# Optimization experiments

Measured on AMD Instinct MI355X. Metric: run time of the kernel, lower is better.

Reference implementation:

```python
import jax, jax.numpy as jnp
import numpy as np

NUM_HEAD = 16
FEAT_DIM = 1024
HEAD_DIM = FEAT_DIM // NUM_HEAD  # 64
MAX_SEQ_LEN = 2048
BATCH = 2


def setup_inputs() -> dict:
    key = jax.random.key(0)
    ks = jax.random.split(key, 6)
    x = jax.random.normal(ks[0], (BATCH, MAX_SEQ_LEN, FEAT_DIM), dtype=jnp.float32)
    # xavier_uniform: limit = sqrt(6/(fan_in+fan_out)); torch Linear weight is [out, in]
    def xavier(k, out_f, in_f):
        lim = float(np.sqrt(6.0 / (in_f + out_f)))
        return jax.random.uniform(k, (out_f, in_f), dtype=jnp.float32, minval=-lim, maxval=lim)
    W1 = xavier(ks[1], HEAD_DIM, HEAD_DIM)          # attn_mlp[0].weight
    b1 = jnp.zeros((HEAD_DIM,), dtype=jnp.float32)
    W2 = xavier(ks[2], MAX_SEQ_LEN, HEAD_DIM)       # attn_mlp[2].weight
    b2 = jnp.zeros((MAX_SEQ_LEN,), dtype=jnp.float32)
    Wv = xavier(ks[3], FEAT_DIM, FEAT_DIM)          # value_linear.weight (no bias)
    Wo = xavier(ks[4], FEAT_DIM, FEAT_DIM)          # output_linear.weight (no bias)
    return {"x": x, "W1": W1, "b1": b1, "W2": W2, "b2": b2, "Wv": Wv, "Wo": Wo}


def _split_head(t):
    b, n, _ = t.shape
    return t.reshape(b, n, NUM_HEAD, HEAD_DIM).transpose(0, 2, 1, 3)  # [b,h,n,d]


def reference(x, W1, b1, W2, b2, Wv, Wo):
    # value projection (dropout is identity in eval / p=0)
    value = x @ Wv.T                                   # [b,n,F]
    vh = _split_head(value)                            # [b,h,n,d]
    xh = _split_head(x)                                # [b,h,n,d]
    # per-head MLP -> dense attention logits [b,h,n,max_seq_len]
    hid = jax.nn.relu(jnp.einsum('bhnd,ed->bhne', xh, W1) + b1)
    logits = jnp.einsum('bhne,me->bhnm', hid, W2) + b2
    attn = jax.nn.softmax(logits, axis=-1)             # [b,h,n,m]
    out_h = jnp.einsum('bhnm,bhmd->bhnd', attn, vh)    # m == seq_len
    b_, h_, n_, d_ = out_h.shape
    out = out_h.transpose(0, 2, 1, 3).reshape(b_, n_, FEAT_DIM)
    return out @ Wo.T
```

## Files before the change

kernel.cpp:

```cpp
#include <hip/hip_runtime.h>
#include <hip/hip_bf16.h>
#include <math.h>
#include <stdint.h>


typedef __attribute__((ext_vector_type(8))) short bf16x8;
typedef __attribute__((ext_vector_type(4))) float f32x4;

#define LOG2E 1.4426950408889634f

__device__ __forceinline__ unsigned short f2bf(float f) {
  union { float f; unsigned u; } v; v.f = f;
  unsigned r = v.u + 0x7FFFu + ((v.u >> 16) & 1u);
  return (unsigned short)(r >> 16);
}

__global__ __launch_bounds__(256) void conv_bf16(const float* __restrict__ src,
                                                 unsigned short* __restrict__ dst, int nq) {
  int stride = gridDim.x * blockDim.x;
  for (int q = blockIdx.x * blockDim.x + threadIdx.x; q < nq; q += stride) {
    float4 v = *(const float4*)(src + (size_t)q * 4);
    unsigned short p0 = f2bf(v.x), p1 = f2bf(v.y), p2 = f2bf(v.z), p3 = f2bf(v.w);
    uint2 u;
    u.x = (unsigned)p0 | ((unsigned)p1 << 16);
    u.y = (unsigned)p2 | ((unsigned)p3 << 16);
    *(uint2*)(dst + (size_t)q * 4) = u;
  }
}

__global__ __launch_bounds__(256) void b2l_kernel(const float* __restrict__ src,
                                                  float* __restrict__ dst, int n) {
  int i = blockIdx.x * blockDim.x + threadIdx.x;
  if (i < n) dst[i] = src[i] * LOG2E;
}

__device__ __forceinline__ void stage64(const char* g, size_t ldbytes, char* lds,
                                        int w, int lane) {
#pragma unroll
  for (int t = 0; t < 2; ++t) {
    int row  = w * 16 + t * 8 + (lane >> 3);
    int csrc = (lane & 7) ^ (lane >> 3);
    const char* src = g + (size_t)row * ldbytes + (csrc << 4);
    char* dst = lds + ((w * 2 + t) << 10);
    __builtin_amdgcn_global_load_lds((const __attribute__((address_space(1))) void*)src,
                                     (__attribute__((address_space(3))) void*)dst,
                                     16, 0, 0);
  }
}

__device__ __forceinline__ bf16x8 rdfrag(const char* lds, int row, int kt, int lane) {
  int c = ((kt << 2) + (lane >> 4)) ^ (row & 7);
  return *(const bf16x8*)(lds + row * 128 + (c << 4));
}

template<int MODE>
__global__ __launch_bounds__(256) void gemm_bt(const unsigned short* __restrict__ A,
                                               const unsigned short* __restrict__ B,
                                               void* __restrict__ C, int K) {
  __shared__ __attribute__((aligned(16))) char As[8192];
  __shared__ __attribute__((aligned(16))) char Bs[8192];
  int tid = threadIdx.x, w = tid >> 6, lane = tid & 63;
  int bm = blockIdx.x, bn = blockIdx.y;
  const char* Ab = (const char*)A + (size_t)bm * 64 * (K * 2);
  const char* Bb = (const char*)B + (size_t)bn * 64 * (K * 2);
  f32x4 acc[4] = {};
  int nsteps = K >> 6;
  for (int kk = 0; kk < nsteps; ++kk) {
    __syncthreads();
    stage64(Ab + (size_t)kk * 128, (size_t)K * 2, As, w, lane);
    stage64(Bb + (size_t)kk * 128, (size_t)K * 2, Bs, w, lane);
    __syncthreads();
#pragma unroll
    for (int kt = 0; kt < 2; ++kt) {
      bf16x8 a = rdfrag(As, w * 16 + (lane & 15), kt, lane);
#pragma unroll
      for (int nj = 0; nj < 4; ++nj) {
        bf16x8 b = rdfrag(Bs, nj * 16 + (lane & 15), kt, lane);
        acc[nj] = __builtin_amdgcn_mfma_f32_16x16x32_bf16(a, b, acc[nj], 0, 0, 0);
      }
    }
  }
  int g = lane >> 4, fr = lane & 15;
  if (MODE == 0) {
    unsigned short* vt = (unsigned short*)C;
    int growbase = bm * 64 + w * 16 + g * 4;
    int b = growbase >> 11;
    int n = growbase & 2047;
#pragma unroll
    for (int nj = 0; nj < 4; ++nj) {
      int d = nj * 16 + fr;
      unsigned short p0 = f2bf(acc[nj][0]), p1 = f2bf(acc[nj][1]);
      unsigned short p2 = f2bf(acc[nj][2]), p3 = f2bf(acc[nj][3]);
      uint2 u;
      u.x = (unsigned)p0 | ((unsigned)p1 << 16);
      u.y = (unsigned)p2 | ((unsigned)p3 << 16);
      *(uint2*)(vt + ((size_t)((b * 16 + bn) * 64 + d)) * 2048 + n) = u;
    }
  } else {
    float* Cf = (float*)C;
    int grow = bm * 64 + w * 16 + g * 4;
#pragma unroll
    for (int nj = 0; nj < 4; ++nj) {
#pragma unroll
      for (int r = 0; r < 4; ++r) {
        Cf[(size_t)(grow + r) * 1024 + bn * 64 + nj * 16 + fr] = acc[nj][r];
      }
    }
  }
}

__global__ __launch_bounds__(256) void flash_kernel(const unsigned short* __restrict__ xb,
                                                    const unsigned short* __restrict__ w1b,
                                                    const float* __restrict__ b1,
                                                    const unsigned short* __restrict__ w2b,
                                                    const float* __restrict__ b2l,
                                                    const unsigned short* __restrict__ vt,
                                                    unsigned short* __restrict__ aout) {
  __shared__ __attribute__((aligned(16))) char Ks[2][8192];
  __shared__ __attribute__((aligned(16))) char Vs[2][8192];
  __shared__ __attribute__((aligned(16))) char Qs[8192];
  int tid = threadIdx.x, w = tid >> 6, lane = tid & 63;
  int qt = blockIdx.x, bh = blockIdx.y;
  int b = bh >> 4, h = bh & 15;
  int g = lane >> 4, fr = lane & 15;

  stage64((const char*)(xb + ((size_t)(b * 2048 + qt * 64)) * 1024 + h * 64), 2048, Ks[0], w, lane);
  stage64((const char*)w1b, 128, Vs[0], w, lane);
  __syncthreads();
  {
    f32x4 hq[4] = {};
#pragma unroll
    for (int kt = 0; kt < 2; ++kt) {
      bf16x8 a = rdfrag(Ks[0], w * 16 + fr, kt, lane);
#pragma unroll
      for (int j = 0; j < 4; ++j) {
        bf16x8 bw = rdfrag(Vs[0], j * 16 + fr, kt, lane);
        hq[j] = __builtin_amdgcn_mfma_f32_16x16x32_bf16(a, bw, hq[j], 0, 0, 0);
      }
    }
#pragma unroll
    for (int r = 0; r < 4; ++r) {
      int row = w * 16 + g * 4 + r;
      int swz = (row & 7) << 4;
#pragma unroll
      for (int j = 0; j < 4; ++j) {
        float v = fmaxf(hq[j][r] + b1[j * 16 + fr], 0.f) * LOG2E;
        int byteoff = (row << 7) + ((((j << 4) + fr) << 1) ^ swz);
        *(unsigned short*)(Qs + byteoff) = f2bf(v);
      }
    }
  }
  bf16x8 qf0 = rdfrag(Qs, w * 16 + fr, 0, lane);
  bf16x8 qf1 = rdfrag(Qs, w * 16 + fr, 1, lane);
  __syncthreads();

  const char* vtb = (const char*)vt + (size_t)bh * 64 * 4096;
  stage64((const char*)w2b, 128, Ks[0], w, lane);
  stage64(vtb, 4096, Vs[0], w, lane);

  bf16x8 ones;
#pragma unroll
  for (int i = 0; i < 8; ++i) ones[i] = (short)0x3F80;

  f32x4 o[4] = {};
  f32x4 o1 = {};
  char* myPs = Qs + (w << 11);
  int cur = 0;
  int swz = (fr & 7) << 4;

  float4 e4a[4];
#pragma unroll
  for (int j = 0; j < 4; ++j) e4a[j] = *(const float4*)(b2l + j * 16 + g * 4);

  __syncthreads();

  for (int mt = 0; mt < 32; ++mt) {
    if (mt < 31) {
      stage64((const char*)w2b + (size_t)(mt + 1) * 8192, 128, Ks[cur ^ 1], w, lane);
      stage64(vtb + (size_t)(mt + 1) * 128, 4096, Vs[cur ^ 1], w, lane);
    }

    f32x4 s[4];
#pragma unroll
    for (int j = 0; j < 4; ++j) {
      s[j] = (f32x4){e4a[j].x, e4a[j].y, e4a[j].z, e4a[j].w};
      bf16x8 kb0 = rdfrag(Ks[cur], j * 16 + fr, 0, lane);
      s[j] = __builtin_amdgcn_mfma_f32_16x16x32_bf16(kb0, qf0, s[j], 0, 0, 0);
      bf16x8 kb1 = rdfrag(Ks[cur], j * 16 + fr, 1, lane);
      s[j] = __builtin_amdgcn_mfma_f32_16x16x32_bf16(kb1, qf1, s[j], 0, 0, 0);
    }
    if (mt < 31) {
#pragma unroll
      for (int j = 0; j < 4; ++j)
        e4a[j] = *(const float4*)(b2l + (mt + 1) * 64 + j * 16 + g * 4);
    }

#pragma unroll
    for (int j = 0; j < 4; ++j) {
      float p0, p1, p2, p3;
      asm("v_exp_f32 %0, %1" : "=v"(p0) : "v"(s[j][0]));
      asm("v_exp_f32 %0, %1" : "=v"(p1) : "v"(s[j][1]));
      asm("v_exp_f32 %0, %1" : "=v"(p2) : "v"(s[j][2]));
      asm("v_exp_f32 %0, %1" : "=v"(p3) : "v"(s[j][3]));
      unsigned ux, uy;
      asm("v_cvt_pk_bf16_f32 %0, %1, %2" : "=v"(ux) : "v"(p0), "v"(p1));
      asm("v_cvt_pk_bf16_f32 %0, %1, %2" : "=v"(uy) : "v"(p2), "v"(p3));
      uint2 u; u.x = ux; u.y = uy;
      int byteoff = (fr << 7) + (((j << 5) + (g << 3)) ^ swz);
      *(uint2*)(myPs + byteoff) = u;
    }

#pragma unroll
    for (int kt = 0; kt < 2; ++kt) {
      bf16x8 pf = rdfrag(myPs, fr, kt, lane);
      o1 = __builtin_amdgcn_mfma_f32_16x16x32_bf16(pf, ones, o1, 0, 0, 0);
#pragma unroll
      for (int dj = 0; dj < 4; ++dj) {
        bf16x8 vb = rdfrag(Vs[cur], dj * 16 + fr, kt, lane);
        o[dj] = __builtin_amdgcn_mfma_f32_16x16x32_bf16(pf, vb, o[dj], 0, 0, 0);
      }
    }
    __syncthreads();
    cur ^= 1;
  }

  float invr[4];
#pragma unroll
  for (int r = 0; r < 4; ++r) invr[r] = 1.f / o1[r];
  int nbase = qt * 64 + w * 16 + g * 4;
#pragma unroll
  for (int dj = 0; dj < 4; ++dj) {
    int f = h * 64 + dj * 16 + fr;
#pragma unroll
    for (int r = 0; r < 4; ++r) {
      aout[((size_t)(b * 2048 + nbase + r)) * 1024 + f] = f2bf(o[dj][r] * invr[r]);
    }
  }
}

extern "C" void kernel_launch(void* const* d_in, const int* in_sizes, int n_in,
                              void* d_out, int out_size, void* d_ws, size_t ws_size,
                              hipStream_t stream) {
  (void)in_sizes; (void)n_in; (void)out_size; (void)ws_size;
  const float* x  = (const float*)d_in[0];
  const float* W1 = (const float*)d_in[1];
  const float* b1 = (const float*)d_in[2];
  const float* W2 = (const float*)d_in[3];
  const float* b2 = (const float*)d_in[4];
  const float* Wv = (const float*)d_in[5];
  const float* Wo = (const float*)d_in[6];
  float* out = (float*)d_out;

  char* ws = (char*)d_ws;
  unsigned short* xb   = (unsigned short*)(ws);
  unsigned short* wvb  = (unsigned short*)(ws +  8388608);
  unsigned short* wob  = (unsigned short*)(ws + 10485760);
  unsigned short* w2b  = (unsigned short*)(ws + 12582912);
  unsigned short* w1b  = (unsigned short*)(ws + 12845056);
  float*          b2l  = (float*)         (ws + 12853248);
  unsigned short* vt   = (unsigned short*)(ws + 21233664);
  unsigned short* aout = (unsigned short*)(ws + 29622272);

  conv_bf16<<<1024, 256, 0, stream>>>(x,  xb,  4194304 / 4);
  conv_bf16<<<1024, 256, 0, stream>>>(Wv, wvb, 1048576 / 4);
  conv_bf16<<<1024, 256, 0, stream>>>(Wo, wob, 1048576 / 4);
  conv_bf16<<< 128, 256, 0, stream>>>(W2, w2b,  131072 / 4);
  conv_bf16<<<   4, 256, 0, stream>>>(W1, w1b,    4096 / 4);
  b2l_kernel<<<   8, 256, 0, stream>>>(b2, b2l, 2048);

  gemm_bt<0><<<dim3(64, 16), 256, 0, stream>>>(xb, wvb, (void*)vt, 1024);
  flash_kernel<<<dim3(32, 32), 256, 0, stream>>>(xb, w1b, b1, w2b, b2l, vt, aout);
  gemm_bt<1><<<dim3(64, 16), 256, 0, stream>>>(aout, wob, (void*)out, 1024);
}
```

Measured before the change: 113.7 us.

## Rewrite attention kernel with 32x32 MFMA, 128-row query tiles and register P

New measurement: 110.7 us. -2.7%, faster.

```diff
diff --git a/kernel.cpp b/kernel.cpp
--- a/kernel.cpp
+++ b/kernel.cpp
@@ -6,6 +6,7 @@
 
 typedef __attribute__((ext_vector_type(8))) short bf16x8;
 typedef __attribute__((ext_vector_type(4))) float f32x4;
+typedef __attribute__((ext_vector_type(16))) float f32x16;
 
 #define LOG2E 1.4426950408889634f
 
@@ -51,6 +52,35 @@
 __device__ __forceinline__ bf16x8 rdfrag(const char* lds, int row, int kt, int lane) {
   int c = ((kt << 2) + (lane >> 4)) ^ (row & 7);
   return *(const bf16x8*)(lds + row * 128 + (c << 4));
+}
+
+__device__ __forceinline__ bf16x8 rdfrag32(const char* lds, int row, int chunk) {
+  int c = chunk ^ (row & 7);
+  return *(const bf16x8*)(lds + row * 128 + (c << 4));
+}
+
+__device__ __forceinline__ f32x16 loadb16(const float* p) {
+  f32x16 r;
+#pragma unroll
+  for (int qd = 0; qd < 4; ++qd) {
+    float4 v = *(const float4*)(p + qd * 8);
+    r[qd * 4 + 0] = v.x; r[qd * 4 + 1] = v.y; r[qd * 4 + 2] = v.z; r[qd * 4 + 3] = v.w;
+  }
+  return r;
+}
+
+__device__ __forceinline__ bf16x8 pk_swap(float r0, float r1, float r2, float r3,
+                                          float r4, float r5, float r6, float r7) {
+  unsigned a, b, c, d;
+  asm("v_cvt_pk_bf16_f32 %0, %1, %2" : "=v"(a) : "v"(r0), "v"(r1));
+  asm("v_cvt_pk_bf16_f32 %0, %1, %2" : "=v"(b) : "v"(r4), "v"(r5));
+  asm("v_cvt_pk_bf16_f32 %0, %1, %2" : "=v"(c) : "v"(r2), "v"(r3));
+  asm("v_cvt_pk_bf16_f32 %0, %1, %2" : "=v"(d) : "v"(r6), "v"(r7));
+  asm("v_permlane32_swap_b32 %0, %1" : "+v"(a), "+v"(b));
+  asm("v_permlane32_swap_b32 %0, %1" : "+v"(c), "+v"(d));
+  union { unsigned u[4]; bf16x8 v; } r;
+  r.u[0] = a; r.u[1] = c; r.u[2] = b; r.u[3] = d;
+  return r.v;
 }
 
 template<int MODE>
@@ -116,125 +146,126 @@
                                                     const float* __restrict__ b2l,
                                                     const unsigned short* __restrict__ vt,
                                                     unsigned short* __restrict__ aout) {
-  __shared__ __attribute__((aligned(16))) char Ks[2][8192];
-  __shared__ __attribute__((aligned(16))) char Vs[2][8192];
-  __shared__ __attribute__((aligned(16))) char Qs[8192];
+  __shared__ __attribute__((aligned(16))) char Kbuf[16384];
+  __shared__ __attribute__((aligned(16))) char Vbuf[16384];
   int tid = threadIdx.x, w = tid >> 6, lane = tid & 63;
-  int qt = blockIdx.x, bh = blockIdx.y;
+  int l31 = lane & 31, hi = lane >> 5;
+  int f = blockIdx.x;
+  int swz = ((f & 7) << 6) | (f >> 3);
+  int qt = swz & 15, bh = swz >> 4;
   int b = bh >> 4, h = bh & 15;
-  int g = lane >> 4, fr = lane & 15;
-
-  stage64((const char*)(xb + ((size_t)(b * 2048 + qt * 64)) * 1024 + h * 64), 2048, Ks[0], w, lane);
-  stage64((const char*)w1b, 128, Vs[0], w, lane);
+
+  const char* px = (const char*)(xb + ((size_t)(b * 2048 + qt * 128)) * 1024 + h * 64);
+  stage64(px, 2048, Kbuf, w, lane);
+  stage64(px + (size_t)64 * 2048, 2048, Kbuf + 8192, w, lane);
+  stage64((const char*)w1b, 128, Vbuf, w, lane);
   __syncthreads();
-  {
-    f32x4 hq[4] = {};
-#pragma unroll
-    for (int kt = 0; kt < 2; ++kt) {
-      bf16x8 a = rdfrag(Ks[0], w * 16 + fr, kt, lane);
-#pragma unroll
-      for (int j = 0; j < 4; ++j) {
-        bf16x8 bw = rdfrag(Vs[0], j * 16 + fr, kt, lane);
-        hq[j] = __builtin_amdgcn_mfma_f32_16x16x32_bf16(a, bw, hq[j], 0, 0, 0);
+
+  f32x16 h0 = loadb16(b1 + hi * 4);
+  f32x16 h1 = loadb16(b1 + 32 + hi * 4);
+#pragma unroll
+  for (int ks = 0; ks < 4; ++ks) {
+    bf16x8 xf = rdfrag32(Kbuf, w * 32 + l31, ks * 2 + hi);
+    bf16x8 wf0 = rdfrag32(Vbuf, l31, ks * 2 + hi);
+    h0 = __builtin_amdgcn_mfma_f32_32x32x16_bf16(wf0, xf, h0, 0, 0, 0);
+    bf16x8 wf1 = rdfrag32(Vbuf, 32 + l31, ks * 2 + hi);
+    h1 = __builtin_amdgcn_mfma_f32_32x32x16_bf16(wf1, xf, h1, 0, 0, 0);
+  }
+#pragma unroll
+  for (int i = 0; i < 16; ++i) {
+    h0[i] = fmaxf(h0[i], 0.f) * LOG2E;
+    h1[i] = fmaxf(h1[i], 0.f) * LOG2E;
+  }
+  bf16x8 qb[4];
+  qb[0] = pk_swap(h0[0], h0[1], h0[2], h0[3], h0[4], h0[5], h0[6], h0[7]);
+  qb[1] = pk_swap(h0[8], h0[9], h0[10], h0[11], h0[12], h0[13], h0[14], h0[15]);
+  qb[2] = pk_swap(h1[0], h1[1], h1[2], h1[3], h1[4], h1[5], h1[6], h1[7]);
+  qb[3] = pk_swap(h1[8], h1[9], h1[10], h1[11], h1[12], h1[13], h1[14], h1[15]);
+  __syncthreads();
+
+  const char* vtb = (const char*)vt + (size_t)bh * 64 * 4096;
+  stage64((const char*)w2b, 128, Kbuf, w, lane);
+  stage64(vtb, 4096, Vbuf, w, lane);
+  float4 pre[8];
+#pragma unroll
+  for (int pq = 0; pq < 4; ++pq) {
+    pre[pq]     = *(const float4*)(b2l + pq * 8 + hi * 4);
+    pre[pq + 4] = *(const float4*)(b2l + 32 + pq * 8 + hi * 4);
+  }
+  f32x16 oA = {}, oB = {};
+  float lrs0 = 0.f, lrs1 = 0.f, lrs2 = 0.f, lrs3 = 0.f;
+  __syncthreads();
+
+  for (int mt = 0; mt < 32; ++mt) {
+    int cur = mt & 1;
+    const char* Kc = Kbuf + (cur << 13);
+    const char* Vc = Vbuf + (cur << 13);
+    if (mt < 31) {
+      stage64((const char*)w2b + (size_t)(mt + 1) * 8192, 128, Kbuf + ((cur ^ 1) << 13), w, lane);
+      stage64(vtb + (size_t)(mt + 1) * 128, 4096, Vbuf + ((cur ^ 1) << 13), w, lane);
+    }
+    f32x16 s0, s1;
+#pragma unroll
+    for (int qd = 0; qd < 4; ++qd) {
+      s0[qd * 4 + 0] = pre[qd].x;     s0[qd * 4 + 1] = pre[qd].y;
+      s0[qd * 4 + 2] = pre[qd].z;     s0[qd * 4 + 3] = pre[qd].w;
+      s1[qd * 4 + 0] = pre[qd + 4].x; s1[qd * 4 + 1] = pre[qd + 4].y;
+      s1[qd * 4 + 2] = pre[qd + 4].z; s1[qd * 4 + 3] = pre[qd + 4].w;
+    }
+#pragma unroll
+    for (int kt = 0; kt < 4; ++kt) {
+      bf16x8 kf0 = rdfrag32(Kc, l31, kt * 2 + hi);
+      s0 = __builtin_amdgcn_mfma_f32_32x32x16_bf16(kf0, qb[kt], s0, 0, 0, 0);
+      bf16x8 kf1 = rdfrag32(Kc, 32 + l31, kt * 2 + hi);
+      s1 = __builtin_amdgcn_mfma_f32_32x32x16_bf16(kf1, qb[kt], s1, 0, 0, 0);
+    }
+    if (mt < 31) {
+#pragma unroll
+      for (int pq = 0; pq < 4; ++pq) {
+        pre[pq]     = *(const float4*)(b2l + (mt + 1) * 64 + pq * 8 + hi * 4);
+        pre[pq + 4] = *(const float4*)(b2l + (mt + 1) * 64 + 32 + pq * 8 + hi * 4);
       }
     }
 #pragma unroll
-    for (int r = 0; r < 4; ++r) {
-      int row = w * 16 + g * 4 + r;
-      int swz = (row & 7) << 4;
-#pragma unroll
-      for (int j = 0; j < 4; ++j) {
-        float v = fmaxf(hq[j][r] + b1[j * 16 + fr], 0.f) * LOG2E;
-        int byteoff = (row << 7) + ((((j << 4) + fr) << 1) ^ swz);
-        *(unsigned short*)(Qs + byteoff) = f2bf(v);
-      }
-    }
-  }
-  bf16x8 qf0 = rdfrag(Qs, w * 16 + fr, 0, lane);
-  bf16x8 qf1 = rdfrag(Qs, w * 16 + fr, 1, lane);
-  __syncthreads();
-
-  const char* vtb = (const char*)vt + (size_t)bh * 64 * 4096;
-  stage64((const char*)w2b, 128, Ks[0], w, lane);
-  stage64(vtb, 4096, Vs[0], w, lane);
-
-  bf16x8 ones;
-#pragma unroll
-  for (int i = 0; i < 8; ++i) ones[i] = (short)0x3F80;
-
-  f32x4 o[4] = {};
-  f32x4 o1 = {};
-  char* myPs = Qs + (w << 11);
-  int cur = 0;
-  int swz = (fr & 7) << 4;
-
-  float4 e4a[4];
-#pragma unroll
-  for (int j = 0; j < 4; ++j) e4a[j] = *(const float4*)(b2l + j * 16 + g * 4);
-
-  __syncthreads();
-
-  for (int mt = 0; mt < 32; ++mt) {
-    if (mt < 31) {
-      stage64((const char*)w2b + (size_t)(mt + 1) * 8192, 128, Ks[cur ^ 1], w, lane);
-      stage64(vtb + (size_t)(mt + 1) * 128, 4096, Vs[cur ^ 1], w, lane);
-    }
-
-    f32x4 s[4];
-#pragma unroll
-    for (int j = 0; j < 4; ++j) {
-      s[j] = (f32x4){e4a[j].x, e4a[j].y, e4a[j].z, e4a[j].w};
-      bf16x8 kb0 = rdfrag(Ks[cur], j * 16 + fr, 0, lane);
-      s[j] = __builtin_amdgcn_mfma_f32_16x16x32_bf16(kb0, qf0, s[j], 0, 0, 0);
-      bf16x8 kb1 = rdfrag(Ks[cur], j * 16 + fr, 1, lane);
-      s[j] = __builtin_amdgcn_mfma_f32_16x16x32_bf16(kb1, qf1, s[j], 0, 0, 0);
-    }
-    if (mt < 31) {
-#pragma unroll
-      for (int j = 0; j < 4; ++j)
-        e4a[j] = *(const float4*)(b2l + (mt + 1) * 64 + j * 16 + g * 4);
-    }
-
-#pragma unroll
-    for (int j = 0; j < 4; ++j) {
-      float p0, p1, p2, p3;
-      asm("v_exp_f32 %0, %1" : "=v"(p0) : "v"(s[j][0]));
-      asm("v_exp_f32 %0, %1" : "=v"(p1) : "v"(s[j][1]));
-      asm("v_exp_f32 %0, %1" : "=v"(p2) : "v"(s[j][2]));
-      asm("v_exp_f32 %0, %1" : "=v"(p3) : "v"(s[j][3]));
-      unsigned ux, uy;
-      asm("v_cvt_pk_bf16_f32 %0, %1, %2" : "=v"(ux) : "v"(p0), "v"(p1));
-      asm("v_cvt_pk_bf16_f32 %0, %1, %2" : "=v"(uy) : "v"(p2), "v"(p3));
-      uint2 u; u.x = ux; u.y = uy;
-      int byteoff = (fr << 7) + (((j << 5) + (g << 3)) ^ swz);
-      *(uint2*)(myPs + byteoff) = u;
-    }
-
-#pragma unroll
-    for (int kt = 0; kt < 2; ++kt) {
-      bf16x8 pf = rdfrag(myPs, fr, kt, lane);
-      o1 = __builtin_amdgcn_mfma_f32_16x16x32_bf16(pf, ones, o1, 0, 0, 0);
-#pragma unroll
-      for (int dj = 0; dj < 4; ++dj) {
-        bf16x8 vb = rdfrag(Vs[cur], dj * 16 + fr, kt, lane);
-        o[dj] = __builtin_amdgcn_mfma_f32_16x16x32_bf16(pf, vb, o[dj], 0, 0, 0);
-      }
+    for (int i = 0; i < 16; ++i) {
+      float t0, t1;
+      asm("v_exp_f32 %0, %1" : "=v"(t0) : "v"(s0[i]));
+      asm("v_exp_f32 %0, %1" : "=v"(t1) : "v"(s1[i]));
+      s0[i] = t0; s1[i] = t1;
+      if ((i & 3) == 0) { lrs0 += t0; lrs0 += t1; }
+      else if ((i & 3) == 1) { lrs1 += t0; lrs1 += t1; }
+      else if ((i & 3) == 2) { lrs2 += t0; lrs2 += t1; }
+      else { lrs3 += t0; lrs3 += t1; }
+    }
+    bf16x8 pa[4];
+    pa[0] = pk_swap(s0[0], s0[1], s0[2], s0[3], s0[4], s0[5], s0[6], s0[7]);
+    pa[1] = pk_swap(s0[8], s0[9], s0[10], s0[11], s0[12], s0[13], s0[14], s0[15]);
+    pa[2] = pk_swap(s1[0], s1[1], s1[2], s1[3], s1[4], s1[5], s1[6], s1[7]);
+    pa[3] = pk_swap(s1[8], s1[9], s1[10], s1[11], s1[12], s1[13], s1[14], s1[15]);
+#pragma unroll
+    for (int ks = 0; ks < 4; ++ks) {
+      bf16x8 vf0 = rdfrag32(Vc, l31, ks * 2 + hi);
+      oA = __builtin_amdgcn_mfma_f32_32x32x16_bf16(pa[ks], vf0, oA, 0, 0, 0);
+      bf16x8 vf1 = rdfrag32(Vc, 32 + l31, ks * 2 + hi);
+      oB = __builtin_amdgcn_mfma_f32_32x32x16_bf16(pa[ks], vf1, oB, 0, 0, 0);
     }
     __syncthreads();
-    cur ^= 1;
-  }
-
-  float invr[4];
-#pragma unroll
-  for (int r = 0; r < 4; ++r) invr[r] = 1.f / o1[r];
-  int nbase = qt * 64 + w * 16 + g * 4;
-#pragma unroll
-  for (int dj = 0; dj < 4; ++dj) {
-    int f = h * 64 + dj * 16 + fr;
-#pragma unroll
-    for (int r = 0; r < 4; ++r) {
-      aout[((size_t)(b * 2048 + nbase + r)) * 1024 + f] = f2bf(o[dj][r] * invr[r]);
-    }
+  }
+
+  float l = (lrs0 + lrs1) + (lrs2 + lrs3);
+  l += __shfl_xor(l, 32);
+  float inv = 1.f / l;
+  float iv[16];
+#pragma unroll
+  for (int r = 0; r < 16; ++r)
+    iv[r] = __shfl(inv, (r & 3) + 8 * (r >> 2) + 4 * hi);
+  int nb = qt * 128 + w * 32;
+#pragma unroll
+  for (int r = 0; r < 16; ++r) {
+    int ql = (r & 3) + 8 * (r >> 2) + 4 * hi;
+    size_t off = ((size_t)(b * 2048 + nb + ql)) * 1024 + h * 64 + l31;
+    aout[off]      = f2bf(oA[r] * iv[r]);
+    aout[off + 32] = f2bf(oB[r] * iv[r]);
   }
 }
 
@@ -269,6 +300,6 @@
   b2l_kernel<<<   8, 256, 0, stream>>>(b2, b2l, 2048);
 
   gemm_bt<0><<<dim3(64, 16), 256, 0, stream>>>(xb, wvb, (void*)vt, 1024);
-  flash_kernel<<<dim3(32, 32), 256, 0, stream>>>(xb, w1b, b1, w2b, b2l, vt, aout);
+  flash_kernel<<<512, 256, 0, stream>>>(xb, w1b, b1, w2b, b2l, vt, aout);
   gemm_bt<1><<<dim3(64, 16), 256, 0, stream>>>(aout, wob, (void*)out, 1024);
 }
```
